# Performance work log

Measured on AMD Instinct MI355X. Metric: run time of the kernel, lower is better.

## Reference

```python
import jax, jax.numpy as jnp
import numpy as np

B, L, D, H = 32768, 11, 32, 4
HD = D // H
VOCAB, NPOS, PE = 10000, 16, 16
EPS = 1e-5


def _safe_mask(m):
    # disable padding mask for rows where ALL positions are padding
    all_pad = m.all(axis=1)
    return m & ~all_pad[:, None]


def _aggregate(out, query_mask):
    sm = _safe_mask(query_mask)
    valid = (~sm)[..., None].astype(out.dtype)  # (B, L, 1)
    return (out * valid).sum(axis=1) / jnp.clip(valid.sum(axis=1), 1.0, None)


def _mha(xq, xkv, in_w, in_b, out_w, out_b, kpm):
    # torch nn.MultiheadAttention (batch_first, eval): packed in_proj then out_proj
    Bq, Lq, _ = xq.shape
    Wq, Wk, Wv = jnp.split(in_w, 3, axis=0)
    bq, bk, bv = jnp.split(in_b, 3, axis=0)
    q = (xq @ Wq.T + bq).reshape(Bq, Lq, H, HD)
    k = (xkv @ Wk.T + bk).reshape(Bq, -1, H, HD)
    v = (xkv @ Wv.T + bv).reshape(Bq, -1, H, HD)
    s = jnp.einsum('bqhd,bkhd->bhqk', q, k) / np.sqrt(HD).astype(np.float32)
    s = jnp.where(kpm[:, None, None, :], -jnp.inf, s)
    a = jax.nn.softmax(s, axis=-1)
    o = jnp.einsum('bhqk,bkhd->bqhd', a, v).reshape(Bq, Lq, D)
    return o @ out_w.T + out_b


def setup_inputs() -> dict:
    key = jax.random.key(0)
    ks = jax.random.split(key, 14)
    inp = {
        'home_players': jax.random.randint(ks[0], (B, L), 0, VOCAB),
        'away_players': jax.random.randint(ks[1], (B, L), 0, VOCAB),
        'h_positions': jax.random.randint(ks[2], (B, L), 0, NPOS),
        'a_positions': jax.random.randint(ks[3], (B, L), 0, NPOS),
        'emb': jax.random.normal(ks[4], (VOCAB, PE), jnp.float32) * 0.02,
        'pos_emb': jax.random.normal(ks[5], (NPOS, PE), jnp.float32) * 0.02,
        'h2a_in_w': jax.random.normal(ks[6], (3 * D, D), jnp.float32) * 0.05,
        'h2a_in_b': jnp.zeros((3 * D,), jnp.float32),
        'h2a_out_w': jax.random.normal(ks[7], (D, D), jnp.float32) * 0.05,
        'h2a_out_b': jnp.zeros((D,), jnp.float32),
        'a2h_in_w': jax.random.normal(ks[8], (3 * D, D), jnp.float32) * 0.05,
        'a2h_in_b': jnp.zeros((3 * D,), jnp.float32),
        'a2h_out_w': jax.random.normal(ks[9], (D, D), jnp.float32) * 0.05,
        'a2h_out_b': jnp.zeros((D,), jnp.float32),
        'gate_w': jax.random.normal(ks[10], (D, 2 * D), jnp.float32) * 0.05,
        'gate_b': jnp.zeros((D,), jnp.float32),
        'ln_w': jnp.ones((D,), jnp.float32),
        'ln_b': jnp.zeros((D,), jnp.float32),
    }
    return inp


def reference(home_players, away_players, h_positions, a_positions,
              emb, pos_emb,
              h2a_in_w, h2a_in_b, h2a_out_w, h2a_out_b,
              a2h_in_w, a2h_in_b, a2h_out_w, a2h_out_b,
              gate_w, gate_b, ln_w, ln_b):
    h_vecs = jnp.concatenate([emb[home_players], pos_emb[h_positions]], axis=-1)  # (B,L,D)
    a_vecs = jnp.concatenate([emb[away_players], pos_emb[a_positions]], axis=-1)
    h_mask = home_players == 0
    a_mask = away_players == 0
    h2a_out = _mha(h_vecs, a_vecs, h2a_in_w, h2a_in_b, h2a_out_w, h2a_out_b, _safe_mask(a_mask))
    h2a_vec = _aggregate(h2a_out, h_mask)
    a2h_out = _mha(a_vecs, h_vecs, a2h_in_w, a2h_in_b, a2h_out_w, a2h_out_b, _safe_mask(h_mask))
    a2h_vec = _aggregate(a2h_out, a_mask)
    concat = jnp.concatenate([h2a_vec, a2h_vec], axis=1)
    gate = jax.nn.sigmoid(concat @ gate_w.T + gate_b)
    matchup = gate * h2a_vec + (1.0 - gate) * a2h_vec
    mu = matchup.mean(axis=-1, keepdims=True)
    var = ((matchup - mu) ** 2).mean(axis=-1, keepdims=True)
    return (matchup - mu) / jnp.sqrt(var + EPS) * ln_w + ln_b
```

## Files before the change

kernel.cpp:

```cpp
#include <hip/hip_runtime.h>
#include <hip/hip_bf16.h>

typedef unsigned int u32;
typedef unsigned short u16;
typedef short bf16x8 __attribute__((ext_vector_type(8)));
typedef float f32x4 __attribute__((ext_vector_type(4)));

#define LQ 11
#define RPB 8
#define NR 88

__device__ __forceinline__ float blo(u32 x) { return __uint_as_float(x << 16); }
__device__ __forceinline__ float bhi(u32 x) { return __uint_as_float(x & 0xFFFF0000u); }
__device__ __forceinline__ float bf1(u16 x) { return __uint_as_float(((u32)x) << 16); }
__device__ __forceinline__ u16 f2b(float f) {
    __hip_bfloat16 h = __float2bfloat16(f);
    return *reinterpret_cast<u16*>(&h);
}
__device__ __forceinline__ u32 pk2(float a, float b) {
    return (u32)f2b(a) | ((u32)f2b(b) << 16);
}

__global__ __launch_bounds__(512, 6)
void CrossTeam_v9(const int* __restrict__ home, const int* __restrict__ away,
                  const int* __restrict__ hpos, const int* __restrict__ apos,
                  const float* __restrict__ emb, const float* __restrict__ pemb,
                  const float* __restrict__ h2a_w, const float* __restrict__ h2a_b,
                  const float* __restrict__ h2a_ow, const float* __restrict__ h2a_ob,
                  const float* __restrict__ a2h_w, const float* __restrict__ a2h_b,
                  const float* __restrict__ a2h_ow, const float* __restrict__ a2h_ob,
                  const float* __restrict__ gw, const float* __restrict__ gb,
                  const float* __restrict__ lnw, const float* __restrict__ lnb,
                  float* __restrict__ out)
{
    __shared__ u16 proj[6][NR * 32];
    __shared__ union {
        int ptab[2][NR][2];
        struct {
            float obuf[2][RPB][32];
            float ybuf[2][RPB][32];
        } cd;
    } u;
    __shared__ u32 mraw[2][RPB];

    const int t = threadIdx.x;
    const int b0 = blockIdx.x * RPB;

    if (t < 176) {
        const int side = t / 88;
        const int s = t - side * 88;
        const int r = s / 11, l = s - r * 11;
        const int gi = (b0 + r) * LQ + l;
        u.ptab[side][s][0] = side ? away[gi] : home[gi];
        u.ptab[side][s][1] = side ? apos[gi] : hpos[gi];
    }
    if (t >= 496) {
        const int k = t - 496; const int side = k >> 3; const int r = k & 7;
        const int* arr = side ? away : home;
        u32 m = 0;
        for (int l = 0; l < LQ; ++l) m |= (u32)(arr[(b0 + r) * LQ + l] == 0) << l;
        mraw[side][r] = m;
    }
    __syncthreads();

    const int wave = t >> 6, lane = t & 63;
    const int lq = lane >> 4, lm = lane & 15;

    {
        const int side = wave >> 2;
        const int mh = (wave >> 1) & 1;
        const int nh = wave & 1;
        const float* wq_src  = side ? a2h_w : h2a_w;
        const float* wkv_src = side ? h2a_w : a2h_w;
        const float* bq_src  = side ? a2h_b : h2a_b;
        const float* bkv_src = side ? h2a_b : a2h_b;
        bf16x8 afrag[3]; float bias[3][4];
        #pragma unroll
        for (int i = 0; i < 3; ++i) {
            const int M = (mh * 3 + i) * 16;
            const float* ws = (M < 32) ? wq_src : wkv_src;
            const float* wp = ws + (M + lm) * 32 + lq * 8;
            const f32x4 a0 = *(const f32x4*)wp;
            const f32x4 a1 = *(const f32x4*)(wp + 4);
            union { bf16x8 v; u32 w[4]; } au;
            au.w[0] = pk2(a0[0], a0[1]); au.w[1] = pk2(a0[2], a0[3]);
            au.w[2] = pk2(a1[0], a1[1]); au.w[3] = pk2(a1[2], a1[3]);
            afrag[i] = au.v;
            const float* bs = (M < 32) ? bq_src : bkv_src;
            #pragma unroll
            for (int j = 0; j < 4; ++j) bias[i][j] = bs[M + lq * 4 + j];
        }
        bf16x8 bfrag[3];
        #pragma unroll
        for (int nn = 0; nn < 3; ++nn) {
            const int srow = (nh * 3 + nn) * 16 + lm;
            const int s = srow < NR ? srow : NR - 1;
            const int id = u.ptab[side][s][lq >> 1];
            const float* gp = ((lq < 2) ? emb : pemb) + id * 16 + (lq & 1) * 8;
            const f32x4 g0 = *(const f32x4*)gp;
            const f32x4 g1 = *(const f32x4*)(gp + 4);
            union { bf16x8 v; u32 w[4]; } bu;
            bu.w[0] = pk2(g0[0], g0[1]); bu.w[1] = pk2(g0[2], g0[3]);
            bu.w[2] = pk2(g1[0], g1[1]); bu.w[3] = pk2(g1[2], g1[3]);
            bfrag[nn] = bu.v;
        }
        #pragma unroll
        for (int nn = 0; nn < 3; ++nn) {
            const int srow = (nh * 3 + nn) * 16 + lm;
            #pragma unroll
            for (int i = 0; i < 3; ++i) {
                f32x4 acc = { bias[i][0], bias[i][1], bias[i][2], bias[i][3] };
                acc = __builtin_amdgcn_mfma_f32_16x16x32_bf16(afrag[i], bfrag[nn], acc, 0, 0, 0);
                const int mt = mh * 3 + i;
                const int mat = side * 3 + (mt >> 1);
                const int dimw = (mt & 1) * 16 + lq * 4;
                if (srow < NR) {
                    const int phys = srow * 32 + ((((dimw >> 3) ^ srow) & 3) << 3) + (dimw & 7);
                    uint2 pk;
                    pk.x = pk2(acc[0], acc[1]);
                    pk.y = pk2(acc[2], acc[3]);
                    *(uint2*)&proj[mat][phys] = pk;
                }
            }
        }
    }
    __syncthreads();

    {
        const int hh = lane >> 4;
        const int slot = lane & 15;
        const int qi = slot < 11 ? slot : 10;
        const int dpv = hh * 8 + (slot & 7);
        #pragma unroll
        for (int it = 0; it < 2; ++it) {
            const int task = wave * 2 + it;
            const int r = task >> 1, dir = task & 1;
            const int qmat = dir ? 3 : 0;
            const int kmat = dir ? 1 : 4;
            const int vmat = dir ? 2 : 5;
            const int r11 = r * 11;
            const u32 kvraw = mraw[dir ? 0 : 1][r];
            const u32 kv = (kvraw == 0x7FFu) ? 0u : kvraw;
            const u32 qraw = mraw[dir ? 1 : 0][r];
            const u32 smq = (qraw == 0x7FFu) ? 0u : qraw;
            const u32 vm = (~smq) & 0x7FFu;
            const float invc = 1.0f / (float)__popc(vm);
            const float wqw = (slot < 11 && ((vm >> slot) & 1u)) ? invc : 0.f;
            const int qrow = r11 + qi;
            const uint4 qp = *(const uint4*)&proj[qmat][qrow * 32 + (((hh ^ qrow) & 3) << 3)];
            float qv[8];
            qv[0]=blo(qp.x); qv[1]=bhi(qp.x); qv[2]=blo(qp.y); qv[3]=bhi(qp.y);
            qv[4]=blo(qp.z); qv[5]=bhi(qp.z); qv[6]=blo(qp.w); qv[7]=bhi(qp.w);
            float e[11]; float sum = 0.f;
            #pragma unroll
            for (int ki = 0; ki < 11; ++ki) {
                const int krow = r11 + ki;
                const uint4 kp = *(const uint4*)&proj[kmat][krow * 32 + (((hh ^ krow) & 3) << 3)];
                float s = qv[0]*blo(kp.x) + qv[1]*bhi(kp.x) + qv[2]*blo(kp.y) + qv[3]*bhi(kp.y)
                        + qv[4]*blo(kp.z) + qv[5]*bhi(kp.z) + qv[6]*blo(kp.w) + qv[7]*bhi(kp.w);
                s *= 0.35355339059327373f;
                e[ki] = ((kv >> ki) & 1u) ? 0.f : __expf(s);
                sum += e[ki];
            }
            const float rs = wqw / fmaxf(sum, 1e-20f);
            float o = 0.f;
            #pragma unroll
            for (int ki = 0; ki < 11; ++ki) {
                float v = e[ki] * rs;
                v += __shfl_xor(v, 1, 16);
                v += __shfl_xor(v, 2, 16);
                v += __shfl_xor(v, 4, 16);
                v += __shfl_xor(v, 8, 16);
                const int vrow = r11 + ki;
                const float vv = bf1(proj[vmat][vrow * 32 + (((hh ^ vrow) & 3) << 3) + (slot & 7)]);
                o += v * vv;
            }
            if (slot < 8) u.cd.obuf[dir][r][dpv] = o;
        }
    }
    __syncthreads();

    if (t < 256) {
        const int r = t >> 5, d = t & 31;
        float yh = h2a_ob[d];
        const float* wr = h2a_ow + d * 32;
        #pragma unroll
        for (int c = 0; c < 32; ++c) yh += u.cd.obuf[0][r][c] * wr[c];
        float ya = a2h_ob[d];
        wr = a2h_ow + d * 32;
        #pragma unroll
        for (int c = 0; c < 32; ++c) ya += u.cd.obuf[1][r][c] * wr[c];
        u.cd.ybuf[0][r][d] = yh; u.cd.ybuf[1][r][d] = ya;
        float acc = gb[d];
        const float* gr = gw + d * 64;
        #pragma unroll
        for (int c = 0; c < 32; ++c) acc += u.cd.ybuf[0][r][c] * gr[c];
        #pragma unroll
        for (int c = 0; c < 32; ++c) acc += u.cd.ybuf[1][r][c] * gr[32 + c];
        const float g = 1.0f / (1.0f + __expf(-acc));
        const float m = g * yh + (1.0f - g) * ya;
        float s1 = m, s2 = m * m;
        #pragma unroll
        for (int off = 1; off < 32; off <<= 1) {
            s1 += __shfl_xor(s1, off, 32);
            s2 += __shfl_xor(s2, off, 32);
        }
        const float mu = s1 * 0.03125f;
        const float var = fmaxf(s2 * 0.03125f - mu * mu, 0.f);
        const float res = (m - mu) * rsqrtf(var + 1e-5f) * lnw[d] + lnb[d];
        out[(b0 + r) * 32 + d] = res;
    }
}

extern "C" void kernel_launch(void* const* d_in, const int* in_sizes, int n_in,
                              void* d_out, int out_size, void* d_ws, size_t ws_size,
                              hipStream_t stream) {
    (void)in_sizes; (void)n_in; (void)d_ws; (void)ws_size; (void)out_size;
    CrossTeam_v9<<<32768 / RPB, 512, 0, stream>>>(
        (const int*)d_in[0], (const int*)d_in[1], (const int*)d_in[2], (const int*)d_in[3],
        (const float*)d_in[4], (const float*)d_in[5],
        (const float*)d_in[6], (const float*)d_in[7], (const float*)d_in[8], (const float*)d_in[9],
        (const float*)d_in[10], (const float*)d_in[11], (const float*)d_in[12], (const float*)d_in[13],
        (const float*)d_in[14], (const float*)d_in[15], (const float*)d_in[16], (const float*)d_in[17],
        (float*)d_out);
}
```

Measured before the change: 195.1 us.

## Pre-pack embedding and projection weights to bf16 in workspace, vectorize epilogue

Adds a small pre-pass kernel that converts the embedding table, position table and both in-projection weight matrices to bf16 in the workspace each call. The main kernel then loads MFMA fragments directly as 16-byte bf16 vectors instead of loading fp32 and packing per thread, which halves gather bytes and drops conversion ALU. The epilogue dot products are rewritten with float4 loads. A fallback kernel keeps the old path if the workspace is too small. The cost is an extra launch and a pass over a roughly 660 KB table every call.

```diff
diff --git a/kernel.cpp b/kernel.cpp
--- a/kernel.cpp
+++ b/kernel.cpp
@@ -9,6 +9,12 @@
 #define LQ 11
 #define RPB 8
 #define NR 88
+
+#define EMB_OFF   0
+#define PEMB_OFF  160000
+#define H2AW_OFF  160256
+#define A2HW_OFF  163328
+#define PACK_N    166400
 
 __device__ __forceinline__ float blo(u32 x) { return __uint_as_float(x << 16); }
 __device__ __forceinline__ float bhi(u32 x) { return __uint_as_float(x & 0xFFFF0000u); }
@@ -21,17 +27,32 @@
     return (u32)f2b(a) | ((u32)f2b(b) << 16);
 }
 
+__global__ __launch_bounds__(256)
+void pack_tables(const float* __restrict__ emb, const float* __restrict__ pemb,
+                 const float* __restrict__ h2a_w, const float* __restrict__ a2h_w,
+                 u16* __restrict__ ws)
+{
+    const int i = blockIdx.x * 256 + threadIdx.x;
+    if (i >= PACK_N) return;
+    const float* src; int off;
+    if (i < PEMB_OFF)      { src = emb;   off = EMB_OFF; }
+    else if (i < H2AW_OFF) { src = pemb;  off = PEMB_OFF; }
+    else if (i < A2HW_OFF) { src = h2a_w; off = H2AW_OFF; }
+    else                   { src = a2h_w; off = A2HW_OFF; }
+    ws[i] = f2b(src[i - off]);
+}
+
 __global__ __launch_bounds__(512, 6)
-void CrossTeam_v9(const int* __restrict__ home, const int* __restrict__ away,
-                  const int* __restrict__ hpos, const int* __restrict__ apos,
-                  const float* __restrict__ emb, const float* __restrict__ pemb,
-                  const float* __restrict__ h2a_w, const float* __restrict__ h2a_b,
-                  const float* __restrict__ h2a_ow, const float* __restrict__ h2a_ob,
-                  const float* __restrict__ a2h_w, const float* __restrict__ a2h_b,
-                  const float* __restrict__ a2h_ow, const float* __restrict__ a2h_ob,
-                  const float* __restrict__ gw, const float* __restrict__ gb,
-                  const float* __restrict__ lnw, const float* __restrict__ lnb,
-                  float* __restrict__ out)
+void CrossTeam_v10(const int* __restrict__ home, const int* __restrict__ away,
+                   const int* __restrict__ hpos, const int* __restrict__ apos,
+                   const u16* __restrict__ wsb,
+                   const float* __restrict__ h2a_b,
+                   const float* __restrict__ h2a_ow, const float* __restrict__ h2a_ob,
+                   const float* __restrict__ a2h_b,
+                   const float* __restrict__ a2h_ow, const float* __restrict__ a2h_ob,
+                   const float* __restrict__ gw, const float* __restrict__ gb,
+                   const float* __restrict__ lnw, const float* __restrict__ lnb,
+                   float* __restrict__ out)
 {
     __shared__ u16 proj[6][NR * 32];
     __shared__ union {
@@ -70,22 +91,16 @@
         const int side = wave >> 2;
         const int mh = (wave >> 1) & 1;
         const int nh = wave & 1;
-        const float* wq_src  = side ? a2h_w : h2a_w;
-        const float* wkv_src = side ? h2a_w : a2h_w;
+        const u16* wq_src  = wsb + (side ? A2HW_OFF : H2AW_OFF);
+        const u16* wkv_src = wsb + (side ? H2AW_OFF : A2HW_OFF);
         const float* bq_src  = side ? a2h_b : h2a_b;
         const float* bkv_src = side ? h2a_b : a2h_b;
         bf16x8 afrag[3]; float bias[3][4];
         #pragma unroll
         for (int i = 0; i < 3; ++i) {
             const int M = (mh * 3 + i) * 16;
-            const float* ws = (M < 32) ? wq_src : wkv_src;
-            const float* wp = ws + (M + lm) * 32 + lq * 8;
-            const f32x4 a0 = *(const f32x4*)wp;
-            const f32x4 a1 = *(const f32x4*)(wp + 4);
-            union { bf16x8 v; u32 w[4]; } au;
-            au.w[0] = pk2(a0[0], a0[1]); au.w[1] = pk2(a0[2], a0[3]);
-            au.w[2] = pk2(a1[0], a1[1]); au.w[3] = pk2(a1[2], a1[3]);
-            afrag[i] = au.v;
+            const u16* wsrc = (M < 32) ? wq_src : wkv_src;
+            afrag[i] = *(const bf16x8*)(wsrc + (M + lm) * 32 + lq * 8);
             const float* bs = (M < 32) ? bq_src : bkv_src;
             #pragma unroll
             for (int j = 0; j < 4; ++j) bias[i][j] = bs[M + lq * 4 + j];
@@ -96,13 +111,8 @@
             const int srow = (nh * 3 + nn) * 16 + lm;
             const int s = srow < NR ? srow : NR - 1;
             const int id = u.ptab[side][s][lq >> 1];
-            const float* gp = ((lq < 2) ? emb : pemb) + id * 16 + (lq & 1) * 8;
-            const f32x4 g0 = *(const f32x4*)gp;
-            const f32x4 g1 = *(const f32x4*)(gp + 4);
-            union { bf16x8 v; u32 w[4]; } bu;
-            bu.w[0] = pk2(g0[0], g0[1]); bu.w[1] = pk2(g0[2], g0[3]);
-            bu.w[2] = pk2(g1[0], g1[1]); bu.w[3] = pk2(g1[2], g1[3]);
-            bfrag[nn] = bu.v;
+            bfrag[nn] = *(const bf16x8*)
+                (wsb + ((lq < 2) ? EMB_OFF : PEMB_OFF) + id * 16 + (lq & 1) * 8);
         }
         #pragma unroll
         for (int nn = 0; nn < 3; ++nn) {
@@ -182,6 +192,188 @@
 
     if (t < 256) {
         const int r = t >> 5, d = t & 31;
+        float yh = h2a_ob[d], ya = a2h_ob[d];
+        {
+            const f32x4* w0 = (const f32x4*)(h2a_ow + d * 32);
+            const f32x4* w1 = (const f32x4*)(a2h_ow + d * 32);
+            const f32x4* o0 = (const f32x4*)&u.cd.obuf[0][r][0];
+            const f32x4* o1 = (const f32x4*)&u.cd.obuf[1][r][0];
+            #pragma unroll
+            for (int c = 0; c < 8; ++c) {
+                const f32x4 a = o0[c], b = w0[c], p = o1[c], q = w1[c];
+                yh += a[0]*b[0] + a[1]*b[1] + a[2]*b[2] + a[3]*b[3];
+                ya += p[0]*q[0] + p[1]*q[1] + p[2]*q[2] + p[3]*q[3];
+            }
+        }
+        u.cd.ybuf[0][r][d] = yh; u.cd.ybuf[1][r][d] = ya;
+        float acc = gb[d];
+        {
+            const f32x4* g0 = (const f32x4*)(gw + d * 64);
+            const f32x4* y0 = (const f32x4*)&u.cd.ybuf[0][r][0];
+            const f32x4* y1 = (const f32x4*)&u.cd.ybuf[1][r][0];
+            #pragma unroll
+            for (int c = 0; c < 8; ++c) {
+                const f32x4 a = y0[c], b = g0[c], p = y1[c], q = g0[8 + c];
+                acc += a[0]*b[0] + a[1]*b[1] + a[2]*b[2] + a[3]*b[3];
+                acc += p[0]*q[0] + p[1]*q[1] + p[2]*q[2] + p[3]*q[3];
+            }
+        }
+        const float g = 1.0f / (1.0f + __expf(-acc));
+        const float m = g * yh + (1.0f - g) * ya;
+        float s1 = m, s2 = m * m;
+        #pragma unroll
+        for (int off = 1; off < 32; off <<= 1) {
+            s1 += __shfl_xor(s1, off, 32);
+            s2 += __shfl_xor(s2, off, 32);
+        }
+        const float mu = s1 * 0.03125f;
+        const float var = fmaxf(s2 * 0.03125f - mu * mu, 0.f);
+        const float res = (m - mu) * rsqrtf(var + 1e-5f) * lnw[d] + lnb[d];
+        out[(b0 + r) * 32 + d] = res;
+    }
+}
+
+__global__ __launch_bounds__(512, 6)
+void CrossTeam_v9fb(const int* __restrict__ home, const int* __restrict__ away,
+                    const int* __restrict__ hpos, const int* __restrict__ apos,
+                    const float* __restrict__ emb, const float* __restrict__ pemb,
+                    const float* __restrict__ h2a_w, const float* __restrict__ h2a_b,
+                    const float* __restrict__ h2a_ow, const float* __restrict__ h2a_ob,
+                    const float* __restrict__ a2h_w, const float* __restrict__ a2h_b,
+                    const float* __restrict__ a2h_ow, const float* __restrict__ a2h_ob,
+                    const float* __restrict__ gw, const float* __restrict__ gb,
+                    const float* __restrict__ lnw, const float* __restrict__ lnb,
+                    float* __restrict__ out)
+{
+    __shared__ u16 proj[6][NR * 32];
+    __shared__ union {
+        int ptab[2][NR][2];
+        struct { float obuf[2][RPB][32]; float ybuf[2][RPB][32]; } cd;
+    } u;
+    __shared__ u32 mraw[2][RPB];
+    const int t = threadIdx.x;
+    const int b0 = blockIdx.x * RPB;
+    if (t < 176) {
+        const int side = t / 88, s = t - side * 88;
+        const int r = s / 11, l = s - r * 11;
+        const int gi = (b0 + r) * LQ + l;
+        u.ptab[side][s][0] = side ? away[gi] : home[gi];
+        u.ptab[side][s][1] = side ? apos[gi] : hpos[gi];
+    }
+    if (t >= 496) {
+        const int k = t - 496; const int side = k >> 3; const int r = k & 7;
+        const int* arr = side ? away : home;
+        u32 m = 0;
+        for (int l = 0; l < LQ; ++l) m |= (u32)(arr[(b0 + r) * LQ + l] == 0) << l;
+        mraw[side][r] = m;
+    }
+    __syncthreads();
+    const int wave = t >> 6, lane = t & 63;
+    const int lq = lane >> 4, lm = lane & 15;
+    {
+        const int side = wave >> 2, mh = (wave >> 1) & 1, nh = wave & 1;
+        const float* wq_src  = side ? a2h_w : h2a_w;
+        const float* wkv_src = side ? h2a_w : a2h_w;
+        const float* bq_src  = side ? a2h_b : h2a_b;
+        const float* bkv_src = side ? h2a_b : a2h_b;
+        bf16x8 afrag[3]; float bias[3][4];
+        #pragma unroll
+        for (int i = 0; i < 3; ++i) {
+            const int M = (mh * 3 + i) * 16;
+            const float* ws = (M < 32) ? wq_src : wkv_src;
+            const float* wp = ws + (M + lm) * 32 + lq * 8;
+            const f32x4 a0 = *(const f32x4*)wp;
+            const f32x4 a1 = *(const f32x4*)(wp + 4);
+            union { bf16x8 v; u32 w[4]; } au;
+            au.w[0] = pk2(a0[0], a0[1]); au.w[1] = pk2(a0[2], a0[3]);
+            au.w[2] = pk2(a1[0], a1[1]); au.w[3] = pk2(a1[2], a1[3]);
+            afrag[i] = au.v;
+            const float* bs = (M < 32) ? bq_src : bkv_src;
+            #pragma unroll
+            for (int j = 0; j < 4; ++j) bias[i][j] = bs[M + lq * 4 + j];
+        }
+        bf16x8 bfrag[3];
+        #pragma unroll
+        for (int nn = 0; nn < 3; ++nn) {
+            const int srow = (nh * 3 + nn) * 16 + lm;
+            const int s = srow < NR ? srow : NR - 1;
+            const int id = u.ptab[side][s][lq >> 1];
+            const float* gp = ((lq < 2) ? emb : pemb) + id * 16 + (lq & 1) * 8;
+            const f32x4 g0 = *(const f32x4*)gp;
+            const f32x4 g1 = *(const f32x4*)(gp + 4);
+            union { bf16x8 v; u32 w[4]; } bu;
+            bu.w[0] = pk2(g0[0], g0[1]); bu.w[1] = pk2(g0[2], g0[3]);
+            bu.w[2] = pk2(g1[0], g1[1]); bu.w[3] = pk2(g1[2], g1[3]);
+            bfrag[nn] = bu.v;
+        }
+        #pragma unroll
+        for (int nn = 0; nn < 3; ++nn) {
+            const int srow = (nh * 3 + nn) * 16 + lm;
+            #pragma unroll
+            for (int i = 0; i < 3; ++i) {
+                f32x4 acc = { bias[i][0], bias[i][1], bias[i][2], bias[i][3] };
+                acc = __builtin_amdgcn_mfma_f32_16x16x32_bf16(afrag[i], bfrag[nn], acc, 0, 0, 0);
+                const int mt = mh * 3 + i;
+                const int mat = side * 3 + (mt >> 1);
+                const int dimw = (mt & 1) * 16 + lq * 4;
+                if (srow < NR) {
+                    const int phys = srow * 32 + ((((dimw >> 3) ^ srow) & 3) << 3) + (dimw & 7);
+                    uint2 pk; pk.x = pk2(acc[0], acc[1]); pk.y = pk2(acc[2], acc[3]);
+                    *(uint2*)&proj[mat][phys] = pk;
+                }
+            }
+        }
+    }
+    __syncthreads();
+    {
+        const int hh = lane >> 4, slot = lane & 15;
+        const int qi = slot < 11 ? slot : 10;
+        const int dpv = hh * 8 + (slot & 7);
+        #pragma unroll
+        for (int it = 0; it < 2; ++it) {
+            const int task = wave * 2 + it;
+            const int r = task >> 1, dir = task & 1;
+            const int qmat = dir ? 3 : 0, kmat = dir ? 1 : 4, vmat = dir ? 2 : 5;
+            const int r11 = r * 11;
+            const u32 kvraw = mraw[dir ? 0 : 1][r];
+            const u32 kv = (kvraw == 0x7FFu) ? 0u : kvraw;
+            const u32 qraw = mraw[dir ? 1 : 0][r];
+            const u32 smq = (qraw == 0x7FFu) ? 0u : qraw;
+            const u32 vm = (~smq) & 0x7FFu;
+            const float invc = 1.0f / (float)__popc(vm);
+            const float wqw = (slot < 11 && ((vm >> slot) & 1u)) ? invc : 0.f;
+            const int qrow = r11 + qi;
+            const uint4 qp = *(const uint4*)&proj[qmat][qrow * 32 + (((hh ^ qrow) & 3) << 3)];
+            float qv[8];
+            qv[0]=blo(qp.x); qv[1]=bhi(qp.x); qv[2]=blo(qp.y); qv[3]=bhi(qp.y);
+            qv[4]=blo(qp.z); qv[5]=bhi(qp.z); qv[6]=blo(qp.w); qv[7]=bhi(qp.w);
+            float e[11]; float sum = 0.f;
+            #pragma unroll
+            for (int ki = 0; ki < 11; ++ki) {
+                const int krow = r11 + ki;
+                const uint4 kp = *(const uint4*)&proj[kmat][krow * 32 + (((hh ^ krow) & 3) << 3)];
+                float s = qv[0]*blo(kp.x) + qv[1]*bhi(kp.x) + qv[2]*blo(kp.y) + qv[3]*bhi(kp.y)
+                        + qv[4]*blo(kp.z) + qv[5]*bhi(kp.z) + qv[6]*blo(kp.w) + qv[7]*bhi(kp.w);
+                s *= 0.35355339059327373f;
+                e[ki] = ((kv >> ki) & 1u) ? 0.f : __expf(s);
+                sum += e[ki];
+            }
+            const float rs = wqw / fmaxf(sum, 1e-20f);
+            float o = 0.f;
+            #pragma unroll
+            for (int ki = 0; ki < 11; ++ki) {
+                float v = e[ki] * rs;
+                v += __shfl_xor(v, 1, 16); v += __shfl_xor(v, 2, 16);
+                v += __shfl_xor(v, 4, 16); v += __shfl_xor(v, 8, 16);
+                const int vrow = r11 + ki;
+                o += v * bf1(proj[vmat][vrow * 32 + (((hh ^ vrow) & 3) << 3) + (slot & 7)]);
+            }
+            if (slot < 8) u.cd.obuf[dir][r][dpv] = o;
+        }
+    }
+    __syncthreads();
+    if (t < 256) {
+        const int r = t >> 5, d = t & 31;
         float yh = h2a_ob[d];
         const float* wr = h2a_ow + d * 32;
         #pragma unroll
@@ -202,25 +394,36 @@
         float s1 = m, s2 = m * m;
         #pragma unroll
         for (int off = 1; off < 32; off <<= 1) {
-            s1 += __shfl_xor(s1, off, 32);
-            s2 += __shfl_xor(s2, off, 32);
+            s1 += __shfl_xor(s1, off, 32); s2 += __shfl_xor(s2, off, 32);
         }
         const float mu = s1 * 0.03125f;
         const float var = fmaxf(s2 * 0.03125f - mu * mu, 0.f);
-        const float res = (m - mu) * rsqrtf(var + 1e-5f) * lnw[d] + lnb[d];
-        out[(b0 + r) * 32 + d] = res;
+        out[(b0 + r) * 32 + d] = (m - mu) * rsqrtf(var + 1e-5f) * lnw[d] + lnb[d];
     }
 }
 
 extern "C" void kernel_launch(void* const* d_in, const int* in_sizes, int n_in,
                               void* d_out, int out_size, void* d_ws, size_t ws_size,
                               hipStream_t stream) {
-    (void)in_sizes; (void)n_in; (void)d_ws; (void)ws_size; (void)out_size;
-    CrossTeam_v9<<<32768 / RPB, 512, 0, stream>>>(
-        (const int*)d_in[0], (const int*)d_in[1], (const int*)d_in[2], (const int*)d_in[3],
-        (const float*)d_in[4], (const float*)d_in[5],
-        (const float*)d_in[6], (const float*)d_in[7], (const float*)d_in[8], (const float*)d_in[9],
-        (const float*)d_in[10], (const float*)d_in[11], (const float*)d_in[12], (const float*)d_in[13],
-        (const float*)d_in[14], (const float*)d_in[15], (const float*)d_in[16], (const float*)d_in[17],
-        (float*)d_out);
-}
+    (void)in_sizes; (void)n_in; (void)out_size;
+    if (ws_size >= (size_t)PACK_N * 2) {
+        pack_tables<<<(PACK_N + 255) / 256, 256, 0, stream>>>(
+            (const float*)d_in[4], (const float*)d_in[5],
+            (const float*)d_in[6], (const float*)d_in[10], (u16*)d_ws);
+        CrossTeam_v10<<<32768 / RPB, 512, 0, stream>>>(
+            (const int*)d_in[0], (const int*)d_in[1], (const int*)d_in[2], (const int*)d_in[3],
+            (const u16*)d_ws,
+            (const float*)d_in[7], (const float*)d_in[8], (const float*)d_in[9],
+            (const float*)d_in[11], (const float*)d_in[12], (const float*)d_in[13],
+            (const float*)d_in[14], (const float*)d_in[15], (const float*)d_in[16],
+            (const float*)d_in[17], (float*)d_out);
+    } else {
+        CrossTeam_v9fb<<<32768 / RPB, 512, 0, stream>>>(
+            (const int*)d_in[0], (const int*)d_in[1], (const int*)d_in[2], (const int*)d_in[3],
+            (const float*)d_in[4], (const float*)d_in[5],
+            (const float*)d_in[6], (const float*)d_in[7], (const float*)d_in[8], (const float*)d_in[9],
+            (const float*)d_in[10], (const float*)d_in[11], (const float*)d_in[12], (const float*)d_in[13],
+            (const float*)d_in[14], (const float*)d_in[15], (const float*)d_in[16], (const float*)d_in[17],
+            (float*)d_out);
+    }
+}
```

Result: faster. 180.9 us (-7.3%).
